# Kernel tuning notes

Hardware: AMD Instinct MI355X
Metric: run time of the kernel (lower is better)

Reference implementation:

```python
import jax, jax.numpy as jnp
import numpy as np

D_MODEL = 1024
N_HEADS = 16
WINDOW = 256
SEQ = 4096
BATCH = 1
NEG_INF = -1e30


def setup_inputs() -> dict:
    key = jax.random.key(0)
    ks = jax.random.split(key, 5)
    scale = 0.02
    inp = {"x": jax.random.normal(ks[0], (BATCH, SEQ, D_MODEL), jnp.float32)}
    for i, name in enumerate(["Wq", "Wk", "Wv", "Wo"]):
        inp[name] = jax.random.normal(ks[1 + i], (D_MODEL, D_MODEL), jnp.float32) * scale
    for name in ["bq", "bk", "bv", "bo"]:
        inp[name] = jnp.zeros((D_MODEL,), jnp.float32)
    return inp


def reference(x, Wq, bq, Wk, bk, Wv, bv, Wo, bo):
    B, S, D = x.shape
    H = N_HEADS
    hd = D // H
    # projections (torch Linear == x @ W^T + b; here W is stored pre-transposed)
    q = (x @ Wq + bq).reshape(B, S, H, hd).transpose(0, 2, 1, 3)  # [B,H,S,hd]
    k = (x @ Wk + bk).reshape(B, S, H, hd).transpose(0, 2, 1, 3)
    v = (x @ Wv + bv).reshape(B, S, H, hd).transpose(0, 2, 1, 3)
    scale = 1.0 / jnp.sqrt(jnp.asarray(hd, x.dtype))
    scores = jnp.einsum("bhqd,bhkd->bhqk", q, k) * scale  # [B,H,S,S]
    # causal sliding window: key j visible to query i iff 0 <= i - j < WINDOW
    i = jnp.arange(S)[:, None]
    j = jnp.arange(S)[None, :]
    allowed = (j <= i) & (i - j < WINDOW)  # [S,S]
    scores = jnp.where(allowed, scores, NEG_INF)
    attn = jax.nn.softmax(scores, axis=-1)
    out = jnp.einsum("bhqk,bhkd->bhqd", attn, v)  # [B,H,S,hd]
    out = out.transpose(0, 2, 1, 3).reshape(B, S, D)
    return out @ Wo + bo
```

## Files before the change

### kernel.cpp

```cpp
#include <hip/hip_runtime.h>
#include <hip/hip_bf16.h>


typedef __attribute__((ext_vector_type(8))) short bf16x8;
typedef __attribute__((ext_vector_type(4))) float f32x4;

#define S_LEN 4096
#define D_MODEL 1024
#define N_HEADS 16
#define HEAD_DIM 64
#define WINDOW 256
#define QKV_LD 3072

static __device__ __forceinline__ unsigned short f2bfbits(float f) {
    __hip_bfloat16 h = __float2bfloat16(f);
    unsigned short u;
    __builtin_memcpy(&u, &h, sizeof(u));
    return u;
}

typedef const __attribute__((address_space(1))) void c_gvoid;
typedef __attribute__((address_space(3))) void lvoid;
static __device__ __forceinline__ void gload16(const void* g, void* l) {
    __builtin_amdgcn_global_load_lds((c_gvoid*)g, (lvoid*)l, 16, 0, 0);
}

__global__ __launch_bounds__(256) void prep_k(const float* __restrict__ x,
                                              const float* __restrict__ Wq,
                                              const float* __restrict__ Wk,
                                              const float* __restrict__ Wv,
                                              const float* __restrict__ Wo,
                                              const float* __restrict__ bq,
                                              const float* __restrict__ bk,
                                              const float* __restrict__ bv,
                                              unsigned short* __restrict__ xb,
                                              __hip_bfloat16* __restrict__ Wqkvt,
                                              __hip_bfloat16* __restrict__ Wot,
                                              float* __restrict__ bias_cat) {
    const int b = blockIdx.x;
    const int t = threadIdx.x;
    if (b < 2048) {
        int i = b * 2048 + t * 8;
        float4 v0 = *(const float4*)(x + i);
        float4 v1 = *(const float4*)(x + i + 4);
        ushort4 o0, o1;
        o0.x = f2bfbits(v0.x); o0.y = f2bfbits(v0.y);
        o0.z = f2bfbits(v0.z); o0.w = f2bfbits(v0.w);
        o1.x = f2bfbits(v1.x); o1.y = f2bfbits(v1.y);
        o1.z = f2bfbits(v1.z); o1.w = f2bfbits(v1.w);
        *(ushort4*)(xb + i) = o0;
        *(ushort4*)(xb + i + 4) = o1;
        return;
    }
    if (b < 3072) {
        __shared__ __hip_bfloat16 tile[64][65];
        const int m = (b - 2048) >> 8;
        const int tid = (b - 2048) & 255;
        const int n0 = (tid & 15) * 64, k0 = (tid >> 4) * 64;
        const float* src = (m == 0) ? Wq : (m == 1) ? Wk : (m == 2) ? Wv : Wo;
        __hip_bfloat16* dst = (m < 3) ? (Wqkvt + (size_t)m * D_MODEL * D_MODEL) : Wot;
        for (int c = t; c < 1024; c += 256) {
            int r = c >> 4, c4 = (c & 15) * 4;
            float4 v = *(const float4*)(src + (size_t)(k0 + r) * D_MODEL + n0 + c4);
            tile[r][c4 + 0] = __float2bfloat16(v.x);
            tile[r][c4 + 1] = __float2bfloat16(v.y);
            tile[r][c4 + 2] = __float2bfloat16(v.z);
            tile[r][c4 + 3] = __float2bfloat16(v.w);
        }
        __syncthreads();
        for (int c = t; c < 1024; c += 256) {
            int rr = c >> 4, c4 = (c & 15) * 4;
            ushort4 o;
            unsigned short u0, u1, u2, u3;
            __builtin_memcpy(&u0, &tile[c4 + 0][rr], 2);
            __builtin_memcpy(&u1, &tile[c4 + 1][rr], 2);
            __builtin_memcpy(&u2, &tile[c4 + 2][rr], 2);
            __builtin_memcpy(&u3, &tile[c4 + 3][rr], 2);
            o.x = u0; o.y = u1; o.z = u2; o.w = u3;
            *(ushort4*)((unsigned short*)dst + (size_t)(n0 + rr) * D_MODEL + k0 + c4) = o;
        }
        return;
    }
    for (int c = t; c < 3 * D_MODEL; c += 256) {
        float v = (c < 1024) ? bq[c] : (c < 2048) ? bk[c - 1024] : bv[c - 2048];
        bias_cat[c] = v;
    }
}

__global__ __launch_bounds__(256) void qkv_k(const __hip_bfloat16* __restrict__ A,
                                             const __hip_bfloat16* __restrict__ Bt,
                                             const float* __restrict__ bias,
                                             __hip_bfloat16* __restrict__ Cout) {
    constexpr int K = D_MODEL, N = QKV_LD;
    __shared__ __align__(16) __hip_bfloat16 As[128 * 32];
    __shared__ __align__(16) __hip_bfloat16 Bs[128 * 32];

    const int m0 = blockIdx.y * 128, n0 = blockIdx.x * 128;
    const int t = threadIdx.x;
    const int wave = t >> 6, lane = t & 63;
    const int quad = lane >> 4, l16 = lane & 15;
    const int wm = (wave & 1) * 64, wn = (wave >> 1) * 64;

    const int srow = t >> 2;
    const int scol = (t & 3) * 8;

    f32x4 acc[4][4];
#pragma unroll
    for (int mi = 0; mi < 4; ++mi)
#pragma unroll
        for (int ni = 0; ni < 4; ++ni) acc[mi][ni] = (f32x4){0.f, 0.f, 0.f, 0.f};

    const __hip_bfloat16* gA = A + (size_t)(m0 + srow) * K + scol;
    const __hip_bfloat16* gB = Bt + (size_t)(n0 + srow) * K + scol;
    const size_t strideA = (size_t)64 * K;

    for (int k0 = 0; k0 < K; k0 += 32) {
        gload16(gA + k0, &As[t * 8]);
        gload16(gA + k0 + strideA, &As[2048 + t * 8]);
        gload16(gB + k0, &Bs[t * 8]);
        gload16(gB + k0 + strideA, &Bs[2048 + t * 8]);
        __syncthreads();

        bf16x8 af[4], bfr[4];
#pragma unroll
        for (int mi = 0; mi < 4; ++mi)
            af[mi] = *(const bf16x8*)&As[(wm + mi * 16 + l16) * 32 + quad * 8];
#pragma unroll
        for (int ni = 0; ni < 4; ++ni)
            bfr[ni] = *(const bf16x8*)&Bs[(wn + ni * 16 + l16) * 32 + quad * 8];
#pragma unroll
        for (int mi = 0; mi < 4; ++mi)
#pragma unroll
            for (int ni = 0; ni < 4; ++ni)
                acc[mi][ni] = __builtin_amdgcn_mfma_f32_16x16x32_bf16(
                    af[mi], bfr[ni], acc[mi][ni], 0, 0, 0);
        __syncthreads();
    }

#pragma unroll
    for (int mi = 0; mi < 4; ++mi) {
#pragma unroll
        for (int ni = 0; ni < 4; ++ni) {
#pragma unroll
            for (int r = 0; r < 4; ++r) {
                int row = m0 + wm + mi * 16 + quad * 4 + r;
                int col = n0 + wn + ni * 16 + l16;
                float v = acc[mi][ni][r] + bias[col];
                Cout[(size_t)row * N + col] = __float2bfloat16(v);
            }
        }
    }
}

__global__ __launch_bounds__(256) void wo_k(const __hip_bfloat16* __restrict__ A,
                                            const __hip_bfloat16* __restrict__ Bt,
                                            const float* __restrict__ bias,
                                            float* __restrict__ Cout) {
    constexpr int TM = 128, TN = 64, K = D_MODEL, N = D_MODEL;
    constexpr int MI = 4, NI = 2;
    __shared__ __align__(16) __hip_bfloat16 As[TM * 32];
    __shared__ __align__(16) __hip_bfloat16 Bs[TN * 32];

    const int m0 = blockIdx.y * TM, n0 = blockIdx.x * TN;
    const int t = threadIdx.x;
    const int wave = t >> 6, lane = t & 63;
    const int quad = lane >> 4, l16 = lane & 15;
    const int wm = (wave & 1) * (TM / 2), wn = (wave >> 1) * (TN / 2);

    const int srow = t >> 2;
    const int scol = (t & 3) * 8;

    f32x4 acc[MI][NI];
#pragma unroll
    for (int mi = 0; mi < MI; ++mi)
#pragma unroll
        for (int ni = 0; ni < NI; ++ni) acc[mi][ni] = (f32x4){0.f, 0.f, 0.f, 0.f};

    const __hip_bfloat16* gA = A + (size_t)(m0 + srow) * K + scol;
    const __hip_bfloat16* gB = Bt + (size_t)(n0 + srow) * K + scol;

    for (int k0 = 0; k0 < K; k0 += 32) {
#pragma unroll
        for (int p = 0; p < TM / 64; ++p)
            gload16(gA + (size_t)(p * 64) * K + k0, &As[p * 2048 + t * 8]);
        if (t < 128)
            ;
        gload16(gB + k0, &Bs[t * 8 >= TN * 32 ? 0 : t * 8]);
        __syncthreads();

        bf16x8 af[MI], bfr[NI];
#pragma unroll
        for (int mi = 0; mi < MI; ++mi)
            af[mi] = *(const bf16x8*)&As[(wm + mi * 16 + l16) * 32 + quad * 8];
#pragma unroll
        for (int ni = 0; ni < NI; ++ni)
            bfr[ni] = *(const bf16x8*)&Bs[(wn + ni * 16 + l16) * 32 + quad * 8];
#pragma unroll
        for (int mi = 0; mi < MI; ++mi)
#pragma unroll
            for (int ni = 0; ni < NI; ++ni)
                acc[mi][ni] = __builtin_amdgcn_mfma_f32_16x16x32_bf16(
                    bfr[ni], af[mi], acc[mi][ni], 0, 0, 0);
        __syncthreads();
    }

    float4 bv[NI];
#pragma unroll
    for (int ni = 0; ni < NI; ++ni)
        bv[ni] = *(const float4*)&bias[n0 + wn + ni * 16 + quad * 4];
#pragma unroll
    for (int mi = 0; mi < MI; ++mi) {
        const int row = m0 + wm + mi * 16 + l16;
#pragma unroll
        for (int ni = 0; ni < NI; ++ni) {
            const int col = n0 + wn + ni * 16 + quad * 4;
            float4 o;
            o.x = acc[mi][ni][0] + bv[ni].x;
            o.y = acc[mi][ni][1] + bv[ni].y;
            o.z = acc[mi][ni][2] + bv[ni].z;
            o.w = acc[mi][ni][3] + bv[ni].w;
            *(float4*)(Cout + (size_t)row * N + col) = o;
        }
    }
}

__global__ __launch_bounds__(256) void attn_k(const __hip_bfloat16* __restrict__ QKV,
                                              __hip_bfloat16* __restrict__ AO) {
    __shared__ __align__(16) __hip_bfloat16 Qs[128 * 64];
    __shared__ __align__(16) __hip_bfloat16 Ks[64 * 64];
    __shared__ __align__(16) __hip_bfloat16 Vt[64 * 72];
    __shared__ __align__(16) __hip_bfloat16 Ps[128 * 72];

    const int h = blockIdx.y;
    const int i0 = blockIdx.x * 128;
    const int t = threadIdx.x;
    const int wave = t >> 6, lane = t & 63;
    const int quad = lane >> 4, l16 = lane & 15;
    const float sc = 0.125f * 1.44269504088896f;

    const __hip_bfloat16* Q = QKV + h * HEAD_DIM;
    const __hip_bfloat16* K = QKV + D_MODEL + h * HEAD_DIM;
    const __hip_bfloat16* V = QKV + 2 * D_MODEL + h * HEAD_DIM;

    const int grow = t >> 3;
    const int glog = ((t & 7) ^ ((t >> 3) & 7)) * 8;
#pragma unroll
    for (int p = 0; p < 4; ++p)
        gload16(Q + (size_t)(i0 + p * 32 + grow) * QKV_LD + glog,
                &Qs[p * 2048 + t * 8]);
    __syncthreads();

    const int rq0 = wave * 32 + l16;
    bf16x8 aq[2][2];
#pragma unroll
    for (int m = 0; m < 2; ++m) {
        const int rq = rq0 + m * 16;
#pragma unroll
        for (int kk = 0; kk < 2; ++kk)
            aq[m][kk] = *(const bf16x8*)&Qs[rq * 64 + ((kk * 4 + quad) ^ (rq & 7)) * 8];
    }

    float m_i[2] = {-3.0e38f, -3.0e38f}, l_i[2] = {0.f, 0.f};
    f32x4 Ov[2][4];
#pragma unroll
    for (int m = 0; m < 2; ++m)
#pragma unroll
        for (int no = 0; no < 4; ++no) Ov[m][no] = (f32x4){0.f, 0.f, 0.f, 0.f};

    const int vp = t >> 3, vc = t & 7;

    for (int tt = 0; tt < 6; ++tt) {
        const int tb = i0 - WINDOW + tt * 64;
        if (tb < 0) continue;

#pragma unroll
        for (int p = 0; p < 2; ++p)
            gload16(K + (size_t)(tb + p * 32 + grow) * QKV_LD + glog,
                    &Ks[p * 2048 + t * 8]);
        {
            uint4 v0 = *(const uint4*)(V + (size_t)(tb + 2 * vp) * QKV_LD + vc * 8);
            uint4 v1 = *(const uint4*)(V + (size_t)(tb + 2 * vp + 1) * QKV_LD + vc * 8);
            const unsigned short* a0 = (const unsigned short*)&v0;
            const unsigned short* a1 = (const unsigned short*)&v1;
#pragma unroll
            for (int j = 0; j < 8; ++j) {
                unsigned int pk = (unsigned int)a0[j] | ((unsigned int)a1[j] << 16);
                *(unsigned int*)&Vt[(vc * 8 + j) * 72 + 2 * vp] = pk;
            }
        }
        __syncthreads();

        f32x4 s[2][4];
#pragma unroll
        for (int m = 0; m < 2; ++m)
#pragma unroll
            for (int ni = 0; ni < 4; ++ni) s[m][ni] = (f32x4){0.f, 0.f, 0.f, 0.f};
#pragma unroll
        for (int kk = 0; kk < 2; ++kk)
#pragma unroll
            for (int ni = 0; ni < 4; ++ni) {
                int rk = ni * 16 + l16;
                bf16x8 bk = *(const bf16x8*)&Ks[rk * 64 + ((kk * 4 + quad) ^ (rk & 7)) * 8];
#pragma unroll
                for (int m = 0; m < 2; ++m)
                    s[m][ni] = __builtin_amdgcn_mfma_f32_16x16x32_bf16(
                        bk, aq[m][kk], s[m][ni], 0, 0, 0);
            }

#pragma unroll
        for (int m = 0; m < 2; ++m) {
            const int qi = i0 + rq0 + m * 16;
            float mx = -3.0e38f;
#pragma unroll
            for (int ni = 0; ni < 4; ++ni)
#pragma unroll
                for (int r = 0; r < 4; ++r) {
                    int j = tb + ni * 16 + quad * 4 + r;
                    float v = s[m][ni][r] * sc;
                    bool ok = (j <= qi) && (qi - j < WINDOW);
                    v = ok ? v : -3.0e38f;
                    s[m][ni][r] = v;
                    mx = fmaxf(mx, v);
                }
            mx = fmaxf(mx, __shfl_xor(mx, 16));
            mx = fmaxf(mx, __shfl_xor(mx, 32));
            const float mn = fmaxf(m_i[m], mx);
            const float alpha = exp2f(m_i[m] - mn);
            m_i[m] = mn;
            float sum = 0.f;
#pragma unroll
            for (int ni = 0; ni < 4; ++ni)
#pragma unroll
                for (int r = 0; r < 4; ++r) {
                    float e = exp2f(s[m][ni][r] - mn);
                    s[m][ni][r] = e;
                    sum += e;
                }
            sum += __shfl_xor(sum, 16);
            sum += __shfl_xor(sum, 32);
            l_i[m] = l_i[m] * alpha + sum;
#pragma unroll
            for (int no = 0; no < 4; ++no) Ov[m][no] *= alpha;

            const int rq = rq0 + m * 16;
#pragma unroll
            for (int ni = 0; ni < 4; ++ni) {
                ushort4 w4;
                w4.x = f2bfbits(s[m][ni][0]); w4.y = f2bfbits(s[m][ni][1]);
                w4.z = f2bfbits(s[m][ni][2]); w4.w = f2bfbits(s[m][ni][3]);
                *(ushort4*)&Ps[rq * 72 + ni * 16 + quad * 4] = w4;
            }
        }

#pragma unroll
        for (int kk = 0; kk < 2; ++kk) {
            bf16x8 ap[2];
#pragma unroll
            for (int m = 0; m < 2; ++m)
                ap[m] = *(const bf16x8*)&Ps[(rq0 + m * 16) * 72 + kk * 32 + quad * 8];
#pragma unroll
            for (int no = 0; no < 4; ++no) {
                bf16x8 bvv = *(const bf16x8*)&Vt[(no * 16 + l16) * 72 + kk * 32 + quad * 8];
#pragma unroll
                for (int m = 0; m < 2; ++m)
                    Ov[m][no] = __builtin_amdgcn_mfma_f32_16x16x32_bf16(
                        bvv, ap[m], Ov[m][no], 0, 0, 0);
            }
        }
        __syncthreads();
    }

#pragma unroll
    for (int m = 0; m < 2; ++m) {
        const float inv = 1.0f / l_i[m];
        const int qi = i0 + rq0 + m * 16;
#pragma unroll
        for (int no = 0; no < 4; ++no) {
            ushort4 o;
            o.x = f2bfbits(Ov[m][no][0] * inv);
            o.y = f2bfbits(Ov[m][no][1] * inv);
            o.z = f2bfbits(Ov[m][no][2] * inv);
            o.w = f2bfbits(Ov[m][no][3] * inv);
            *(ushort4*)((unsigned short*)AO + (size_t)qi * D_MODEL + h * HEAD_DIM +
                        no * 16 + quad * 4) = o;
        }
    }
}

extern "C" void kernel_launch(void* const* d_in, const int* in_sizes, int n_in,
                              void* d_out, int out_size, void* d_ws, size_t ws_size,
                              hipStream_t stream) {
    const float* x  = (const float*)d_in[0];
    const float* Wq = (const float*)d_in[1];
    const float* Wk = (const float*)d_in[2];
    const float* Wv = (const float*)d_in[3];
    const float* Wo = (const float*)d_in[4];
    const float* bq = (const float*)d_in[5];
    const float* bk = (const float*)d_in[6];
    const float* bv = (const float*)d_in[7];
    const float* bo = (const float*)d_in[8];
    float* out = (float*)d_out;

    char* w = (char*)d_ws;
    const size_t MB = 1u << 20;
    __hip_bfloat16* xb    = (__hip_bfloat16*)(w + 0 * MB);
    __hip_bfloat16* Wqkvt = (__hip_bfloat16*)(w + 8 * MB);
    __hip_bfloat16* Wot   = (__hip_bfloat16*)(w + 14 * MB);
    float*          bcat  = (float*)(w + 16 * MB);
    __hip_bfloat16* QKV   = (__hip_bfloat16*)(w + 17 * MB);
    __hip_bfloat16* AO    = (__hip_bfloat16*)(w + 41 * MB);

    prep_k<<<3073, 256, 0, stream>>>(x, Wq, Wk, Wv, Wo, bq, bk, bv,
                                     (unsigned short*)xb, Wqkvt, Wot, bcat);

    dim3 gqkv(QKV_LD / 128, S_LEN / 128);
    qkv_k<<<gqkv, 256, 0, stream>>>(xb, Wqkvt, bcat, QKV);

    dim3 ag(S_LEN / 128, N_HEADS);
    attn_k<<<ag, 256, 0, stream>>>(QKV, AO);

    dim3 go(D_MODEL / 64, S_LEN / 128);
    wo_k<<<go, 256, 0, stream>>>(AO, Wot, bo, out);
}
```

Measured before the change: 172.2 us.

## Rewrite QKV projection GEMM as 256x256 double-buffered pipelined kernel

Replaces the 128x128 single-buffered QKV GEMM with a 512-thread kernel computing 256x256 tiles. It uses a 128KB double-buffered LDS with XOR-swizzled layout and interleaves async global-to-LDS loads with MFMA phases via sched barriers, setprio and explicit waitcnt. It also remaps block IDs for L2 locality. The intent is to hide load latency, cut per-k-step barriers and raise arithmetic intensity, at the cost of very high LDS use (one block per CU) and only 192 workgroups, which may underfill the GPU.

```diff
diff --git a/kernel.cpp b/kernel.cpp
--- a/kernel.cpp
+++ b/kernel.cpp
@@ -87,69 +87,136 @@
     }
 }
 
-__global__ __launch_bounds__(256) void qkv_k(const __hip_bfloat16* __restrict__ A,
-                                             const __hip_bfloat16* __restrict__ Bt,
-                                             const float* __restrict__ bias,
-                                             __hip_bfloat16* __restrict__ Cout) {
-    constexpr int K = D_MODEL, N = QKV_LD;
-    __shared__ __align__(16) __hip_bfloat16 As[128 * 32];
-    __shared__ __align__(16) __hip_bfloat16 Bs[128 * 32];
-
-    const int m0 = blockIdx.y * 128, n0 = blockIdx.x * 128;
+__global__ __launch_bounds__(512, 2) void qkv256_k(const __hip_bfloat16* __restrict__ A,
+                                                   const __hip_bfloat16* __restrict__ Bt,
+                                                   const float* __restrict__ bias,
+                                                   __hip_bfloat16* __restrict__ Cout) {
+    __shared__ __align__(16) char lds[131072];
+
+    const int bid = blockIdx.x;
+    const int wg = (bid & 7) * 24 + (bid >> 3);
+    const int by = wg / 12, bx = wg % 12;
+    const int m0 = by * 256, n0 = bx * 256;
+
     const int t = threadIdx.x;
-    const int wave = t >> 6, lane = t & 63;
+    const int w = t >> 6, lane = t & 63;
+    const int wr = w >> 2, wc = w & 3;
     const int quad = lane >> 4, l16 = lane & 15;
-    const int wm = (wave & 1) * 64, wn = (wave >> 1) * 64;
-
-    const int srow = t >> 2;
-    const int scol = (t & 3) * 8;
-
-    f32x4 acc[4][4];
-#pragma unroll
-    for (int mi = 0; mi < 4; ++mi)
-#pragma unroll
-        for (int ni = 0; ni < 4; ++ni) acc[mi][ni] = (f32x4){0.f, 0.f, 0.f, 0.f};
-
-    const __hip_bfloat16* gA = A + (size_t)(m0 + srow) * K + scol;
-    const __hip_bfloat16* gB = Bt + (size_t)(n0 + srow) * K + scol;
-    const size_t strideA = (size_t)64 * K;
-
-    for (int k0 = 0; k0 < K; k0 += 32) {
-        gload16(gA + k0, &As[t * 8]);
-        gload16(gA + k0 + strideA, &As[2048 + t * 8]);
-        gload16(gB + k0, &Bs[t * 8]);
-        gload16(gB + k0 + strideA, &Bs[2048 + t * 8]);
-        __syncthreads();
-
-        bf16x8 af[4], bfr[4];
-#pragma unroll
-        for (int mi = 0; mi < 4; ++mi)
-            af[mi] = *(const bf16x8*)&As[(wm + mi * 16 + l16) * 32 + quad * 8];
-#pragma unroll
-        for (int ni = 0; ni < 4; ++ni)
-            bfr[ni] = *(const bf16x8*)&Bs[(wn + ni * 16 + l16) * 32 + quad * 8];
-#pragma unroll
-        for (int mi = 0; mi < 4; ++mi)
-#pragma unroll
-            for (int ni = 0; ni < 4; ++ni)
-                acc[mi][ni] = __builtin_amdgcn_mfma_f32_16x16x32_bf16(
-                    af[mi], bfr[ni], acc[mi][ni], 0, 0, 0);
-        __syncthreads();
-    }
-
-#pragma unroll
-    for (int mi = 0; mi < 4; ++mi) {
-#pragma unroll
-        for (int ni = 0; ni < 4; ++ni) {
-#pragma unroll
-            for (int r = 0; r < 4; ++r) {
-                int row = m0 + wm + mi * 16 + quad * 4 + r;
-                int col = n0 + wn + ni * 16 + l16;
-                float v = acc[mi][ni][r] + bias[col];
-                Cout[(size_t)row * N + col] = __float2bfloat16(v);
-            }
-        }
-    }
+
+    const int ls = lane >> 3, lc = lane & 7;
+    const int swz = (lc ^ ls) << 3;
+    const __hip_bfloat16* gA = A + (size_t)(m0 + w * 16 + ls) * D_MODEL + swz;
+    const __hip_bfloat16* gB = Bt + (size_t)(n0 + w * 16 + ls) * D_MODEL + swz;
+    const int dbase = w * 2048 + lane * 16;
+
+    const int h3 = l16 & 7;
+    const int colb0 = (quad ^ h3) << 4;
+    const int aoff0 = (wr * 64 + l16) * 128 + colb0;
+    const int aoff1 = aoff0 ^ 64;
+    const int boff0 = 32768 + (wc * 32 + l16) * 128 + colb0;
+    const int boff1 = boff0 ^ 64;
+
+    f32x4 acc[8][4];
+#pragma unroll
+    for (int i = 0; i < 8; ++i)
+#pragma unroll
+        for (int j = 0; j < 4; ++j) acc[i][j] = (f32x4){0.f, 0.f, 0.f, 0.f};
+
+#define ST_A(BUF, KT, HF)                                                      \
+    {                                                                          \
+        const __hip_bfloat16* s_ = gA + (size_t)((HF) * 128) * D_MODEL + (KT) * 64; \
+        char* d_ = lds + ((BUF) * 65536 + (HF) * 16384 + dbase);               \
+        gload16(s_, d_);                                                       \
+        gload16(s_ + 8 * D_MODEL, d_ + 1024);                                  \
+    }
+#define ST_B(BUF, KT, HF)                                                      \
+    {                                                                          \
+        const __hip_bfloat16* s_ = gB + (size_t)((HF) * 128) * D_MODEL + (KT) * 64; \
+        char* d_ = lds + ((BUF) * 65536 + 32768 + (HF) * 16384 + dbase);       \
+        gload16(s_, d_);                                                       \
+        gload16(s_ + 8 * D_MODEL, d_ + 1024);                                  \
+    }
+
+#define PHASE(BUF, MH, NH, STAGE_CODE, TAILWAIT)                               \
+    {                                                                          \
+        __builtin_amdgcn_sched_barrier(0);                                     \
+        bf16x8 a_[4][2], b_[2][2];                                             \
+        const char* ab_ = lds + ((BUF) * 65536 + (MH) * 16384);                \
+        const char* bb_ = lds + ((BUF) * 65536 + (NH) * 16384);                \
+        _Pragma("unroll") for (int i_ = 0; i_ < 4; ++i_) {                     \
+            a_[i_][0] = *(const bf16x8*)(ab_ + aoff0 + i_ * 2048);             \
+            a_[i_][1] = *(const bf16x8*)(ab_ + aoff1 + i_ * 2048);             \
+        }                                                                      \
+        _Pragma("unroll") for (int j_ = 0; j_ < 2; ++j_) {                     \
+            b_[j_][0] = *(const bf16x8*)(bb_ + boff0 + j_ * 2048);             \
+            b_[j_][1] = *(const bf16x8*)(bb_ + boff1 + j_ * 2048);             \
+        }                                                                      \
+        STAGE_CODE;                                                            \
+        TAILWAIT;                                                              \
+        __builtin_amdgcn_sched_barrier(0);                                     \
+        __builtin_amdgcn_s_barrier();                                          \
+        asm volatile("s_waitcnt lgkmcnt(0)" ::: "memory");                     \
+        __builtin_amdgcn_sched_barrier(0);                                     \
+        __builtin_amdgcn_s_setprio(1);                                         \
+        _Pragma("unroll") for (int i_ = 0; i_ < 4; ++i_)                       \
+            _Pragma("unroll") for (int j_ = 0; j_ < 2; ++j_) {                 \
+                acc[(MH) * 4 + i_][(NH) * 2 + j_] =                            \
+                    __builtin_amdgcn_mfma_f32_16x16x32_bf16(                   \
+                        a_[i_][0], b_[j_][0], acc[(MH) * 4 + i_][(NH) * 2 + j_], 0, 0, 0); \
+                acc[(MH) * 4 + i_][(NH) * 2 + j_] =                            \
+                    __builtin_amdgcn_mfma_f32_16x16x32_bf16(                   \
+                        a_[i_][1], b_[j_][1], acc[(MH) * 4 + i_][(NH) * 2 + j_], 0, 0, 0); \
+            }                                                                  \
+        __builtin_amdgcn_s_setprio(0);                                         \
+        __builtin_amdgcn_sched_barrier(0);                                     \
+        __builtin_amdgcn_s_barrier();                                          \
+    }
+
+    ST_A(0, 0, 0); ST_B(0, 0, 0); ST_A(0, 0, 1); ST_B(0, 0, 1);
+    ST_A(1, 1, 0); ST_B(1, 1, 0);
+    asm volatile("s_waitcnt vmcnt(4)" ::: "memory");
+    __builtin_amdgcn_sched_barrier(0);
+    __builtin_amdgcn_s_barrier();
+
+    for (int kt = 0; kt < 16; kt += 2) {
+        const bool g2 = (kt + 2) < 16;
+        const bool g3 = (kt + 3) < 16;
+        PHASE(0, 0, 0, { ST_A(1, kt + 1, 1); }, {});
+        PHASE(0, 0, 1, { ST_B(1, kt + 1, 1); }, {});
+        PHASE(0, 1, 0, { if (g2) ST_A(0, kt + 2, 0); }, {});
+        PHASE(0, 1, 1, { if (g2) ST_B(0, kt + 2, 0); },
+              { if (g2) { asm volatile("s_waitcnt vmcnt(4)" ::: "memory"); }
+                else    { asm volatile("s_waitcnt vmcnt(0)" ::: "memory"); } });
+        PHASE(1, 0, 0, { if (g2) ST_A(0, kt + 2, 1); }, {});
+        PHASE(1, 0, 1, { if (g2) ST_B(0, kt + 2, 1); }, {});
+        PHASE(1, 1, 0, { if (g3) ST_A(1, kt + 3, 0); }, {});
+        PHASE(1, 1, 1, { if (g3) ST_B(1, kt + 3, 0); },
+              { if (g3) { asm volatile("s_waitcnt vmcnt(4)" ::: "memory"); }
+                else    { asm volatile("s_waitcnt vmcnt(0)" ::: "memory"); } });
+    }
+
+#undef PHASE
+#undef ST_A
+#undef ST_B
+
+#pragma unroll
+    for (int mh = 0; mh < 2; ++mh)
+#pragma unroll
+        for (int i = 0; i < 4; ++i) {
+            const int row0 = m0 + mh * 128 + wr * 64 + i * 16 + quad * 4;
+#pragma unroll
+            for (int nh = 0; nh < 2; ++nh)
+#pragma unroll
+                for (int j = 0; j < 2; ++j) {
+                    const int col = n0 + nh * 128 + wc * 32 + j * 16 + l16;
+                    const float bv = bias[col];
+                    const f32x4 v = acc[mh * 4 + i][nh * 2 + j];
+#pragma unroll
+                    for (int r = 0; r < 4; ++r)
+                        Cout[(size_t)(row0 + r) * QKV_LD + col] =
+                            __float2bfloat16(v[r] + bv);
+                }
+        }
 }
 
 __global__ __launch_bounds__(256) void wo_k(const __hip_bfloat16* __restrict__ A,
@@ -413,8 +480,7 @@
     prep_k<<<3073, 256, 0, stream>>>(x, Wq, Wk, Wv, Wo, bq, bk, bv,
                                      (unsigned short*)xb, Wqkvt, Wot, bcat);
 
-    dim3 gqkv(QKV_LD / 128, S_LEN / 128);
-    qkv_k<<<gqkv, 256, 0, stream>>>(xb, Wqkvt, bcat, QKV);
+    qkv256_k<<<192, 512, 0, stream>>>(xb, Wqkvt, bcat, QKV);
 
     dim3 ag(S_LEN / 128, N_HEADS);
     attn_k<<<ag, 256, 0, stream>>>(QKV, AO);
```

New measurement: 176.8 us. 1.03x slower.

## Double-buffer K/V tiles in attention and widen Wo GEMM tile to 128x128

Applied to the files above, without the earlier changes.

The attention kernel now keeps two K/V shared-memory buffers and prefetches the next 64-key tile while computing the current one. This removes one barrier per iteration and hides global load latency, and it raises MFMA priority around the matrix-multiply sections. The output projection GEMM tile grows from 128x64 to 128x128, which halves the block count and increases register use and per-block reuse. The extra LDS and registers could reduce occupancy, and the Wo grid now has only 256 blocks.

```diff
diff --git a/kernel.cpp b/kernel.cpp
--- a/kernel.cpp
+++ b/kernel.cpp
@@ -156,8 +156,8 @@
                                             const __hip_bfloat16* __restrict__ Bt,
                                             const float* __restrict__ bias,
                                             float* __restrict__ Cout) {
-    constexpr int TM = 128, TN = 64, K = D_MODEL, N = D_MODEL;
-    constexpr int MI = 4, NI = 2;
+    constexpr int TM = 128, TN = 128, K = D_MODEL, N = D_MODEL;
+    constexpr int MI = 4, NI = 4;
     __shared__ __align__(16) __hip_bfloat16 As[TM * 32];
     __shared__ __align__(16) __hip_bfloat16 Bs[TN * 32];
 
@@ -165,7 +165,7 @@
     const int t = threadIdx.x;
     const int wave = t >> 6, lane = t & 63;
     const int quad = lane >> 4, l16 = lane & 15;
-    const int wm = (wave & 1) * (TM / 2), wn = (wave >> 1) * (TN / 2);
+    const int wm = (wave & 1) * 64, wn = (wave >> 1) * 64;
 
     const int srow = t >> 2;
     const int scol = (t & 3) * 8;
@@ -178,14 +178,13 @@
 
     const __hip_bfloat16* gA = A + (size_t)(m0 + srow) * K + scol;
     const __hip_bfloat16* gB = Bt + (size_t)(n0 + srow) * K + scol;
+    const size_t stride64 = (size_t)64 * K;
 
     for (int k0 = 0; k0 < K; k0 += 32) {
-#pragma unroll
-        for (int p = 0; p < TM / 64; ++p)
-            gload16(gA + (size_t)(p * 64) * K + k0, &As[p * 2048 + t * 8]);
-        if (t < 128)
-            ;
-        gload16(gB + k0, &Bs[t * 8 >= TN * 32 ? 0 : t * 8]);
+        gload16(gA + k0, &As[t * 8]);
+        gload16(gA + k0 + stride64, &As[2048 + t * 8]);
+        gload16(gB + k0, &Bs[t * 8]);
+        gload16(gB + k0 + stride64, &Bs[2048 + t * 8]);
         __syncthreads();
 
         bf16x8 af[MI], bfr[NI];
@@ -227,8 +226,8 @@
 __global__ __launch_bounds__(256) void attn_k(const __hip_bfloat16* __restrict__ QKV,
                                               __hip_bfloat16* __restrict__ AO) {
     __shared__ __align__(16) __hip_bfloat16 Qs[128 * 64];
-    __shared__ __align__(16) __hip_bfloat16 Ks[64 * 64];
-    __shared__ __align__(16) __hip_bfloat16 Vt[64 * 72];
+    __shared__ __align__(16) __hip_bfloat16 Ks[2][64 * 64];
+    __shared__ __align__(16) __hip_bfloat16 Vt[2][64 * 72];
     __shared__ __align__(16) __hip_bfloat16 Ps[128 * 72];
 
     const int h = blockIdx.y;
@@ -244,10 +243,30 @@
 
     const int grow = t >> 3;
     const int glog = ((t & 7) ^ ((t >> 3) & 7)) * 8;
+    const int vp = t >> 3, vc = t & 7;
+
+    const int tt0 = (i0 >= WINDOW) ? 0 : ((WINDOW - i0) >> 6);
+
 #pragma unroll
     for (int p = 0; p < 4; ++p)
         gload16(Q + (size_t)(i0 + p * 32 + grow) * QKV_LD + glog,
                 &Qs[p * 2048 + t * 8]);
+    {
+        const int tb0 = i0 - WINDOW + tt0 * 64;
+        uint4 pv0 = *(const uint4*)(V + (size_t)(tb0 + 2 * vp) * QKV_LD + vc * 8);
+        uint4 pv1 = *(const uint4*)(V + (size_t)(tb0 + 2 * vp + 1) * QKV_LD + vc * 8);
+#pragma unroll
+        for (int p = 0; p < 2; ++p)
+            gload16(K + (size_t)(tb0 + p * 32 + grow) * QKV_LD + glog,
+                    &Ks[0][p * 2048 + t * 8]);
+        const unsigned short* a0 = (const unsigned short*)&pv0;
+        const unsigned short* a1 = (const unsigned short*)&pv1;
+#pragma unroll
+        for (int j = 0; j < 8; ++j) {
+            unsigned int pk = (unsigned int)a0[j] | ((unsigned int)a1[j] << 16);
+            *(unsigned int*)&Vt[0][(vc * 8 + j) * 72 + 2 * vp] = pk;
+        }
+    }
     __syncthreads();
 
     const int rq0 = wave * 32 + l16;
@@ -267,45 +286,40 @@
 #pragma unroll
         for (int no = 0; no < 4; ++no) Ov[m][no] = (f32x4){0.f, 0.f, 0.f, 0.f};
 
-    const int vp = t >> 3, vc = t & 7;
-
-    for (int tt = 0; tt < 6; ++tt) {
+    for (int tt = tt0; tt < 6; ++tt) {
         const int tb = i0 - WINDOW + tt * 64;
-        if (tb < 0) continue;
-
-#pragma unroll
-        for (int p = 0; p < 2; ++p)
-            gload16(K + (size_t)(tb + p * 32 + grow) * QKV_LD + glog,
-                    &Ks[p * 2048 + t * 8]);
-        {
-            uint4 v0 = *(const uint4*)(V + (size_t)(tb + 2 * vp) * QKV_LD + vc * 8);
-            uint4 v1 = *(const uint4*)(V + (size_t)(tb + 2 * vp + 1) * QKV_LD + vc * 8);
-            const unsigned short* a0 = (const unsigned short*)&v0;
-            const unsigned short* a1 = (const unsigned short*)&v1;
-#pragma unroll
-            for (int j = 0; j < 8; ++j) {
-                unsigned int pk = (unsigned int)a0[j] | ((unsigned int)a1[j] << 16);
-                *(unsigned int*)&Vt[(vc * 8 + j) * 72 + 2 * vp] = pk;
-            }
-        }
-        __syncthreads();
+        const int buf = (tt - tt0) & 1;
 
         f32x4 s[2][4];
 #pragma unroll
         for (int m = 0; m < 2; ++m)
 #pragma unroll
             for (int ni = 0; ni < 4; ++ni) s[m][ni] = (f32x4){0.f, 0.f, 0.f, 0.f};
+        __builtin_amdgcn_s_setprio(1);
 #pragma unroll
         for (int kk = 0; kk < 2; ++kk)
 #pragma unroll
             for (int ni = 0; ni < 4; ++ni) {
                 int rk = ni * 16 + l16;
-                bf16x8 bk = *(const bf16x8*)&Ks[rk * 64 + ((kk * 4 + quad) ^ (rk & 7)) * 8];
+                bf16x8 bk = *(const bf16x8*)&Ks[buf][rk * 64 + ((kk * 4 + quad) ^ (rk & 7)) * 8];
 #pragma unroll
                 for (int m = 0; m < 2; ++m)
                     s[m][ni] = __builtin_amdgcn_mfma_f32_16x16x32_bf16(
                         bk, aq[m][kk], s[m][ni], 0, 0, 0);
             }
+        __builtin_amdgcn_s_setprio(0);
+
+        const bool pf = (tt < 5);
+        uint4 nv0, nv1;
+        if (pf) {
+            const int tbn = tb + 64;
+            nv0 = *(const uint4*)(V + (size_t)(tbn + 2 * vp) * QKV_LD + vc * 8);
+            nv1 = *(const uint4*)(V + (size_t)(tbn + 2 * vp + 1) * QKV_LD + vc * 8);
+#pragma unroll
+            for (int p = 0; p < 2; ++p)
+                gload16(K + (size_t)(tbn + p * 32 + grow) * QKV_LD + glog,
+                        &Ks[buf ^ 1][p * 2048 + t * 8]);
+        }
 
 #pragma unroll
         for (int m = 0; m < 2; ++m) {
@@ -352,6 +366,7 @@
             }
         }
 
+        __builtin_amdgcn_s_setprio(1);
 #pragma unroll
         for (int kk = 0; kk < 2; ++kk) {
             bf16x8 ap[2];
@@ -360,11 +375,22 @@
                 ap[m] = *(const bf16x8*)&Ps[(rq0 + m * 16) * 72 + kk * 32 + quad * 8];
 #pragma unroll
             for (int no = 0; no < 4; ++no) {
-                bf16x8 bvv = *(const bf16x8*)&Vt[(no * 16 + l16) * 72 + kk * 32 + quad * 8];
+                bf16x8 bvv = *(const bf16x8*)&Vt[buf][(no * 16 + l16) * 72 + kk * 32 + quad * 8];
 #pragma unroll
                 for (int m = 0; m < 2; ++m)
                     Ov[m][no] = __builtin_amdgcn_mfma_f32_16x16x32_bf16(
                         bvv, ap[m], Ov[m][no], 0, 0, 0);
+            }
+        }
+        __builtin_amdgcn_s_setprio(0);
+
+        if (pf) {
+            const unsigned short* a0 = (const unsigned short*)&nv0;
+            const unsigned short* a1 = (const unsigned short*)&nv1;
+#pragma unroll
+            for (int j = 0; j < 8; ++j) {
+                unsigned int pk = (unsigned int)a0[j] | ((unsigned int)a1[j] << 16);
+                *(unsigned int*)&Vt[buf ^ 1][(vc * 8 + j) * 72 + 2 * vp] = pk;
             }
         }
         __syncthreads();
@@ -419,6 +445,6 @@
     dim3 ag(S_LEN / 128, N_HEADS);
     attn_k<<<ag, 256, 0, stream>>>(QKV, AO);
 
-    dim3 go(D_MODEL / 64, S_LEN / 128);
+    dim3 go(D_MODEL / 128, S_LEN / 128);
     wo_k<<<go, 256, 0, stream>>>(AO, Wot, bo, out);
 }
```

New measurement: 177.4 us. 3.0% more time.
